# Kernel tuning notes

Hardware: AMD Instinct MI355X
Metric: run time of the kernel (lower is better)

The kernel has to match this reference:

```python
import jax, jax.numpy as jnp
import numpy as np
from jax import lax

ALPHA = 1.5
DIM = -1
N_ITER = 50


def entmax_bisect(x, alpha=ALPHA, dim=DIM, n_iter=N_ITER):
    # alpha == 1.0 would reduce to softmax; alpha is a static Python float here.
    if alpha == 1.0:
        return jax.nn.softmax(x, axis=dim)
    am1 = alpha - 1.0
    z = x - jnp.max(x, axis=dim, keepdims=True)          # max(z) == 0 along dim
    am1_z = am1 * z
    # torch code sorts z and takes the top element; that equals max(z) == 0, so
    # hi = 0 and lo = hi - 1. We compute the max directly (same math, no sort).
    hi = jnp.max(am1_z, axis=dim, keepdims=True)          # == 0
    lo = hi - 1.0

    inv_am1 = 1.0 / am1

    def sum_probs(tau):
        # sum_i max(0, am1*z_i - tau)^{1/am1}, keepdims
        diff = jnp.maximum(am1_z - tau, 0.0)
        return jnp.sum(jnp.power(diff, inv_am1), axis=dim, keepdims=True)

    # The torch version expands lo downward (up to 64 times) until
    # sum_probs(lo) >= 1 everywhere. Since max(am1_z) == hi, at lo = hi - 1 the
    # argmax element alone contributes (hi - lo)^{1/am1} = 1^{1/am1} = 1, so
    # sum_probs(lo) >= 1 always holds and the torch loop breaks on the first
    # iteration without ever modifying lo. We therefore skip it (identical math).

    def bisect_step(carry, _):
        lo, hi = carry
        mid = (lo + hi) * 0.5
        s = sum_probs(mid)
        lo = jnp.where(s > 1.0, mid, lo)
        hi = jnp.where(s <= 1.0, mid, hi)
        return (lo, hi), None

    (lo, hi), _ = lax.scan(bisect_step, (lo, hi), None, length=n_iter)
    tau_star = (lo + hi) * 0.5
    p = jnp.power(jnp.maximum(am1_z - tau_star, 0.0), inv_am1)
    return p / jnp.maximum(jnp.sum(p, axis=dim, keepdims=True), 1e-12)


def setup_inputs() -> dict:
    key = jax.random.key(0)
    x = jax.random.normal(key, (8, 2048, 2048), dtype=jnp.float32)
    return {"x": x}


def reference(x):
    return entmax_bisect(x, alpha=ALPHA, dim=DIM, n_iter=N_ITER)
```

## Files before the change

### kernel.cpp

```cpp
#include <hip/hip_runtime.h>


typedef float f32x4 __attribute__((ext_vector_type(4)));

constexpr int N = 2048;
constexpr int PER_LANE = N / 64;
constexpr int WPB = 4;
constexpr int CAPL = 12;
constexpr int BMAX = 8;
constexpr int K1 = 6;
constexpr int TOTAL_ITER = 50;

__device__ __forceinline__ float wave_sum(float s) {
    #pragma unroll
    for (int off = 32; off >= 1; off >>= 1)
        s += __shfl_xor(s, off, 64);
    return s;
}
__device__ __forceinline__ float wave_max(float m) {
    #pragma unroll
    for (int off = 32; off >= 1; off >>= 1)
        m = fmaxf(m, __shfl_xor(m, off, 64));
    return m;
}

__global__ __launch_bounds__(256, 6)
void entmax15_kernel(const float* __restrict__ x,
                     float* __restrict__ out, int rows) {
    __shared__ float s_cand[WPB][CAPL][64];
    __shared__ float s_bnd[WPB][BMAX];
    __shared__ int   s_cnt[WPB];

    const int wave = threadIdx.x >> 6;
    const int lane = threadIdx.x & 63;
    const int row  = blockIdx.x * WPB + wave;
    if (row >= rows) return;

    const f32x4* xr   = reinterpret_cast<const f32x4*>(x + (size_t)row * N);
    f32x4*       outr = reinterpret_cast<f32x4*>(out + (size_t)row * N);

    float v[PER_LANE];
    #pragma unroll
    for (int c = 0; c < PER_LANE / 4; ++c) {
        f32x4 t = xr[lane + 64 * c];
        v[4*c+0] = t.x; v[4*c+1] = t.y; v[4*c+2] = t.z; v[4*c+3] = t.w;
    }

    float m = v[0];
    #pragma unroll
    for (int i = 1; i < PER_LANE; ++i) m = fmaxf(m, v[i]);
    m = wave_max(m);

    const float nhm = -0.5f * m;
    #pragma unroll
    for (int i = 0; i < PER_LANE; ++i) v[i] = fmaf(0.5f, v[i], nhm);

    #pragma unroll
    for (int k = 0; k < CAPL; ++k) s_cand[wave][k][lane] = -1e30f;
    if (lane < BMAX) s_bnd[wave][lane] = -1e30f;
    if (lane == 0)   s_cnt[wave] = 0;

    int j = 0;
    #pragma unroll
    for (int i = 0; i < PER_LANE; ++i) {
        const bool cand = v[i] > -1.0f;
        const int  slot = (j < CAPL - 1) ? j : (CAPL - 1);
        if (cand) s_cand[wave][slot][lane] = v[i];
        j += cand ? 1 : 0;
    }

    float tau, ssum;
    if (!__any(j > CAPL)) {
        float cd[CAPL];
        #pragma unroll
        for (int k = 0; k < CAPL; ++k) cd[k] = s_cand[wave][k][lane];

        float lo = -1.0f, hi = 0.0f;
        for (int it = 0; it < K1; ++it) {
            const float mid = 0.5f * (lo + hi);
            float sa = 0.f, sb = 0.f;
            #pragma unroll
            for (int k = 0; k < CAPL; k += 2) {
                float d0 = fmaxf(cd[k]   - mid, 0.f);
                float d1 = fmaxf(cd[k+1] - mid, 0.f);
                sa = fmaf(d0, d0, sa);
                sb = fmaf(d1, d1, sb);
            }
            float s = wave_sum(sa + sb);
            if (s > 1.0f) lo = mid; else hi = mid;
        }

        const float cth = hi, lof = lo;
        float nA = 0.f, S1 = 0.f, S2 = 0.f;
        #pragma unroll
        for (int k = 0; k < CAPL; ++k) {
            float u  = cd[k] - cth;
            float um = fmaxf(u, 0.f);
            nA += (u > 0.f) ? 1.0f : 0.0f;
            S1 += um;
            S2  = fmaf(um, um, S2);
            if (u <= 0.f && cd[k] > lof) {
                int t = atomicAdd(&s_cnt[wave], 1);
                if (t < BMAX) s_bnd[wave][t] = cd[k];
            }
        }
        nA = wave_sum(nA); S1 = wave_sum(S1); S2 = wave_sum(S2);

        const int cnt = s_cnt[wave];
        if (cnt <= BMAX) {
            float b0 = s_bnd[wave][0], b1 = s_bnd[wave][1];
            float b2 = s_bnd[wave][2], b3 = s_bnd[wave][3];
            float b4 = s_bnd[wave][4], b5 = s_bnd[wave][5];
            float b6 = s_bnd[wave][6], b7 = s_bnd[wave][7];
            #define CE(a, b) { float _t = fmaxf(a, b); b = fminf(a, b); a = _t; }
            CE(b0,b1) CE(b2,b3) CE(b4,b5) CE(b6,b7)
            CE(b0,b2) CE(b1,b3) CE(b4,b6) CE(b5,b7)
            CE(b1,b2) CE(b5,b6)
            CE(b0,b4) CE(b1,b5) CE(b2,b6) CE(b3,b7)
            CE(b2,b4) CE(b3,b5)
            CE(b1,b2) CE(b3,b4) CE(b5,b6)
            #undef CE
            float nk = nA, S1k = S1, S2k = S2;
            #define STEP(bk) {                                              \
                float t_  = bk - cth;                                       \
                float sc_ = fmaf(t_, fmaf(nk, t_, -2.0f * S1k), S2k);       \
                bool  ac_ = sc_ < 1.0f;                                     \
                float ta_ = ac_ ? t_ : 0.0f;                                \
                nk  += ac_ ? 1.0f : 0.0f;                                   \
                S1k += ta_;                                                 \
                S2k  = fmaf(ta_, ta_, S2k); }
            STEP(b0) STEP(b1) STEP(b2) STEP(b3)
            STEP(b4) STEP(b5) STEP(b6) STEP(b7)
            #undef STEP
            float disc = fmaxf(fmaf(S1k, S1k, -nk * (S2k - 1.0f)), 0.0f);
            tau = cth + (S1k - sqrtf(disc)) / nk;
        } else {
            for (int it = 0; it < TOTAL_ITER - K1; ++it) {
                const float mid = 0.5f * (lo + hi);
                float sa = 0.f, sb = 0.f;
                #pragma unroll
                for (int k = 0; k < CAPL; k += 2) {
                    float d0 = fmaxf(cd[k]   - mid, 0.f);
                    float d1 = fmaxf(cd[k+1] - mid, 0.f);
                    sa = fmaf(d0, d0, sa);
                    sb = fmaf(d1, d1, sb);
                }
                float s = wave_sum(sa + sb);
                if (s > 1.0f) lo = mid; else hi = mid;
            }
            tau = 0.5f * (lo + hi);
        }

        float sa = 0.f, sb = 0.f;
        #pragma unroll
        for (int k = 0; k < CAPL; k += 2) {
            float d0 = fmaxf(cd[k]   - tau, 0.f);
            float d1 = fmaxf(cd[k+1] - tau, 0.f);
            sa = fmaf(d0, d0, sa);
            sb = fmaf(d1, d1, sb);
        }
        ssum = wave_sum(sa + sb);
    } else {
        float lo = -1.0f, hi = 0.0f;
        for (int it = 0; it < TOTAL_ITER; ++it) {
            const float mid = 0.5f * (lo + hi);
            float s0 = 0.f, s1_ = 0.f, s2_ = 0.f, s3_ = 0.f;
            #pragma unroll
            for (int i = 0; i < PER_LANE; i += 4) {
                float d0 = fmaxf(v[i+0] - mid, 0.f);
                float d1 = fmaxf(v[i+1] - mid, 0.f);
                float d2 = fmaxf(v[i+2] - mid, 0.f);
                float d3 = fmaxf(v[i+3] - mid, 0.f);
                s0 = fmaf(d0, d0, s0); s1_ = fmaf(d1, d1, s1_);
                s2_ = fmaf(d2, d2, s2_); s3_ = fmaf(d3, d3, s3_);
            }
            float s = wave_sum((s0 + s1_) + (s2_ + s3_));
            if (s > 1.0f) lo = mid; else hi = mid;
        }
        tau = 0.5f * (lo + hi);
        float s0 = 0.f;
        #pragma unroll
        for (int i = 0; i < PER_LANE; ++i) {
            float d = fmaxf(v[i] - tau, 0.f);
            s0 = fmaf(d, d, s0);
        }
        ssum = wave_sum(s0);
    }

    const float inv = 1.0f / fmaxf(ssum, 1e-12f);
    #pragma unroll
    for (int c = 0; c < PER_LANE / 4; ++c) {
        float d0 = fmaxf(v[4*c+0] - tau, 0.f);
        float d1 = fmaxf(v[4*c+1] - tau, 0.f);
        float d2 = fmaxf(v[4*c+2] - tau, 0.f);
        float d3 = fmaxf(v[4*c+3] - tau, 0.f);
        f32x4 t;
        t.x = (d0 * d0) * inv;
        t.y = (d1 * d1) * inv;
        t.z = (d2 * d2) * inv;
        t.w = (d3 * d3) * inv;
        __builtin_nontemporal_store(t, &outr[lane + 64 * c]);
    }
}

extern "C" void kernel_launch(void* const* d_in, const int* in_sizes, int n_in,
                              void* d_out, int out_size, void* d_ws, size_t ws_size,
                              hipStream_t stream) {
    const float* x = (const float*)d_in[0];
    float* out = (float*)d_out;
    const int rows = in_sizes[0] / N;
    const int blocks = (rows + WPB - 1) / WPB;
    entmax15_kernel<<<blocks, 64 * WPB, 0, stream>>>(x, out, rows);
}
```

Baseline: 57.75 us.

## Process several rows per wave with register prefetch of the next row

Each wave now handles RPW rows strided across the grid and issues the global loads for the next row into registers before solving the current one. The goal is to overlap HBM load latency with the threshold-solve compute, instead of relying only on occupancy. This adds 32 prefetch registers per lane, and launch bounds drop from 6 to 4 blocks per CU, which lowers occupancy. The grid shrinks by a factor of four.

```diff
diff --git a/kernel.cpp b/kernel.cpp
--- a/kernel.cpp
+++ b/kernel.cpp
@@ -6,6 +6,7 @@
 constexpr int N = 2048;
 constexpr int PER_LANE = N / 64;
 constexpr int WPB = 4;
+constexpr int RPW = 4;
 constexpr int CAPL = 12;
 constexpr int BMAX = 8;
 constexpr int K1 = 6;
@@ -24,56 +25,29 @@
     return m;
 }
 
-__global__ __launch_bounds__(256, 6)
-void entmax15_kernel(const float* __restrict__ x,
-                     float* __restrict__ out, int rows) {
-    __shared__ float s_cand[WPB][CAPL][64];
-    __shared__ float s_bnd[WPB][BMAX];
-    __shared__ int   s_cnt[WPB];
-
-    const int wave = threadIdx.x >> 6;
-    const int lane = threadIdx.x & 63;
-    const int row  = blockIdx.x * WPB + wave;
-    if (row >= rows) return;
-
-    const f32x4* xr   = reinterpret_cast<const f32x4*>(x + (size_t)row * N);
-    f32x4*       outr = reinterpret_cast<f32x4*>(out + (size_t)row * N);
-
-    float v[PER_LANE];
-    #pragma unroll
-    for (int c = 0; c < PER_LANE / 4; ++c) {
-        f32x4 t = xr[lane + 64 * c];
-        v[4*c+0] = t.x; v[4*c+1] = t.y; v[4*c+2] = t.z; v[4*c+3] = t.w;
-    }
-
-    float m = v[0];
-    #pragma unroll
-    for (int i = 1; i < PER_LANE; ++i) m = fmaxf(m, v[i]);
-    m = wave_max(m);
-
-    const float nhm = -0.5f * m;
-    #pragma unroll
-    for (int i = 0; i < PER_LANE; ++i) v[i] = fmaf(0.5f, v[i], nhm);
-
-    #pragma unroll
-    for (int k = 0; k < CAPL; ++k) s_cand[wave][k][lane] = -1e30f;
-    if (lane < BMAX) s_bnd[wave][lane] = -1e30f;
-    if (lane == 0)   s_cnt[wave] = 0;
+__device__ __forceinline__ void solve_and_store(
+        float (&v)[PER_LANE], f32x4* __restrict__ outr, int lane,
+        float (&cand)[CAPL][64], float (&bnd)[BMAX], int* cntp) {
+
+    #pragma unroll
+    for (int k = 0; k < CAPL; ++k) cand[k][lane] = -1e30f;
+    if (lane < BMAX) bnd[lane] = -1e30f;
+    if (lane == 0)   *cntp = 0;
 
     int j = 0;
     #pragma unroll
     for (int i = 0; i < PER_LANE; ++i) {
-        const bool cand = v[i] > -1.0f;
+        const bool c = v[i] > -1.0f;
         const int  slot = (j < CAPL - 1) ? j : (CAPL - 1);
-        if (cand) s_cand[wave][slot][lane] = v[i];
-        j += cand ? 1 : 0;
+        if (c) cand[slot][lane] = v[i];
+        j += c ? 1 : 0;
     }
 
     float tau, ssum;
     if (!__any(j > CAPL)) {
         float cd[CAPL];
         #pragma unroll
-        for (int k = 0; k < CAPL; ++k) cd[k] = s_cand[wave][k][lane];
+        for (int k = 0; k < CAPL; ++k) cd[k] = cand[k][lane];
 
         float lo = -1.0f, hi = 0.0f;
         for (int it = 0; it < K1; ++it) {
@@ -100,18 +74,16 @@
             S1 += um;
             S2  = fmaf(um, um, S2);
             if (u <= 0.f && cd[k] > lof) {
-                int t = atomicAdd(&s_cnt[wave], 1);
-                if (t < BMAX) s_bnd[wave][t] = cd[k];
+                int t = atomicAdd(cntp, 1);
+                if (t < BMAX) bnd[t] = cd[k];
             }
         }
         nA = wave_sum(nA); S1 = wave_sum(S1); S2 = wave_sum(S2);
 
-        const int cnt = s_cnt[wave];
+        const int cnt = *cntp;
         if (cnt <= BMAX) {
-            float b0 = s_bnd[wave][0], b1 = s_bnd[wave][1];
-            float b2 = s_bnd[wave][2], b3 = s_bnd[wave][3];
-            float b4 = s_bnd[wave][4], b5 = s_bnd[wave][5];
-            float b6 = s_bnd[wave][6], b7 = s_bnd[wave][7];
+            float b0 = bnd[0], b1 = bnd[1], b2 = bnd[2], b3 = bnd[3];
+            float b4 = bnd[4], b5 = bnd[5], b6 = bnd[6], b7 = bnd[7];
             #define CE(a, b) { float _t = fmaxf(a, b); b = fminf(a, b); a = _t; }
             CE(b0,b1) CE(b2,b3) CE(b4,b5) CE(b6,b7)
             CE(b0,b2) CE(b1,b3) CE(b4,b6) CE(b5,b7)
@@ -203,12 +175,67 @@
     }
 }
 
+__global__ __launch_bounds__(256, 4)
+void entmax15_kernel(const float* __restrict__ x,
+                     float* __restrict__ out, int rows) {
+    __shared__ float s_cand[WPB][CAPL][64];
+    __shared__ float s_bnd[WPB][BMAX];
+    __shared__ int   s_cnt[WPB];
+
+    const int wave = threadIdx.x >> 6;
+    const int lane = threadIdx.x & 63;
+    const int gw   = blockIdx.x * WPB + wave;
+    const int nwaves = gridDim.x * WPB;
+
+    f32x4 pf[8];
+    {
+        const f32x4* xr = reinterpret_cast<const f32x4*>(x + (size_t)gw * N);
+        #pragma unroll
+        for (int c = 0; c < 8; ++c) pf[c] = xr[lane + 64 * c];
+    }
+
+    #pragma unroll
+    for (int k = 0; k < RPW; ++k) {
+        const int row = gw + k * nwaves;
+        if (row >= rows) return;
+
+        float m = fmaxf(fmaxf(pf[0].x, pf[0].y), fmaxf(pf[0].z, pf[0].w));
+        #pragma unroll
+        for (int c = 1; c < 8; ++c)
+            m = fmaxf(m, fmaxf(fmaxf(pf[c].x, pf[c].y), fmaxf(pf[c].z, pf[c].w)));
+        m = wave_max(m);
+
+        const float nhm = -0.5f * m;
+        float v[PER_LANE];
+        #pragma unroll
+        for (int c = 0; c < 8; ++c) {
+            v[4*c+0] = fmaf(0.5f, pf[c].x, nhm);
+            v[4*c+1] = fmaf(0.5f, pf[c].y, nhm);
+            v[4*c+2] = fmaf(0.5f, pf[c].z, nhm);
+            v[4*c+3] = fmaf(0.5f, pf[c].w, nhm);
+        }
+
+        if (k + 1 < RPW) {
+            const int nrow = gw + (k + 1) * nwaves;
+            if (nrow < rows) {
+                const f32x4* xr = reinterpret_cast<const f32x4*>(x + (size_t)nrow * N);
+                #pragma unroll
+                for (int c = 0; c < 8; ++c) pf[c] = xr[lane + 64 * c];
+            }
+        }
+
+        f32x4* outr = reinterpret_cast<f32x4*>(out + (size_t)row * N);
+        solve_and_store(v, outr, lane, s_cand[wave], s_bnd[wave], &s_cnt[wave]);
+    }
+}
+
 extern "C" void kernel_launch(void* const* d_in, const int* in_sizes, int n_in,
                               void* d_out, int out_size, void* d_ws, size_t ws_size,
                               hipStream_t stream) {
     const float* x = (const float*)d_in[0];
     float* out = (float*)d_out;
     const int rows = in_sizes[0] / N;
-    const int blocks = (rows + WPB - 1) / WPB;
+    const int nwaves = (rows + RPW - 1) / RPW;
+    const int blocks = (nwaves + WPB - 1) / WPB;
     entmax15_kernel<<<blocks, 64 * WPB, 0, stream>>>(x, out, rows);
 }
```

Result: slower. 72.62 us (+25.7%).

## Process two rows per wavefront to interleave independent reductions

Applied to the files above, without the earlier changes.

Each wavefront now handles two rows, interleaving their loads, max reductions, candidate bisection, shuffle reductions and stores so the two independent dependency chains can hide each other's latency. Launch bounds drop from 6 to 4 blocks per CU to make room for the doubled register footprint, and the nontemporal stores become ordinary stores. If either row overflows the candidate buffer, both rows take the full 50-iteration fallback. This risks register pressure and lower occupancy, and it assumes an even row count.

```diff
diff --git a/kernel.cpp b/kernel.cpp
--- a/kernel.cpp
+++ b/kernel.cpp
@@ -17,177 +17,33 @@
         s += __shfl_xor(s, off, 64);
     return s;
 }
-__device__ __forceinline__ float wave_max(float m) {
-    #pragma unroll
-    for (int off = 32; off >= 1; off >>= 1)
-        m = fmaxf(m, __shfl_xor(m, off, 64));
-    return m;
-}
-
-__global__ __launch_bounds__(256, 6)
-void entmax15_kernel(const float* __restrict__ x,
-                     float* __restrict__ out, int rows) {
-    __shared__ float s_cand[WPB][CAPL][64];
-    __shared__ float s_bnd[WPB][BMAX];
-    __shared__ int   s_cnt[WPB];
-
-    const int wave = threadIdx.x >> 6;
-    const int lane = threadIdx.x & 63;
-    const int row  = blockIdx.x * WPB + wave;
-    if (row >= rows) return;
-
-    const f32x4* xr   = reinterpret_cast<const f32x4*>(x + (size_t)row * N);
-    f32x4*       outr = reinterpret_cast<f32x4*>(out + (size_t)row * N);
-
-    float v[PER_LANE];
-    #pragma unroll
-    for (int c = 0; c < PER_LANE / 4; ++c) {
-        f32x4 t = xr[lane + 64 * c];
-        v[4*c+0] = t.x; v[4*c+1] = t.y; v[4*c+2] = t.z; v[4*c+3] = t.w;
-    }
-
-    float m = v[0];
-    #pragma unroll
-    for (int i = 1; i < PER_LANE; ++i) m = fmaxf(m, v[i]);
-    m = wave_max(m);
-
-    const float nhm = -0.5f * m;
-    #pragma unroll
-    for (int i = 0; i < PER_LANE; ++i) v[i] = fmaf(0.5f, v[i], nhm);
-
-    #pragma unroll
-    for (int k = 0; k < CAPL; ++k) s_cand[wave][k][lane] = -1e30f;
-    if (lane < BMAX) s_bnd[wave][lane] = -1e30f;
-    if (lane == 0)   s_cnt[wave] = 0;
-
-    int j = 0;
+
+__device__ __forceinline__ void full_solve_store(
+        float (&v)[PER_LANE], f32x4* __restrict__ outr, int lane) {
+    float lo = -1.0f, hi = 0.0f;
+    for (int it = 0; it < TOTAL_ITER; ++it) {
+        const float mid = 0.5f * (lo + hi);
+        float s0 = 0.f, s1 = 0.f, s2 = 0.f, s3 = 0.f;
+        #pragma unroll
+        for (int i = 0; i < PER_LANE; i += 4) {
+            float d0 = fmaxf(v[i+0] - mid, 0.f);
+            float d1 = fmaxf(v[i+1] - mid, 0.f);
+            float d2 = fmaxf(v[i+2] - mid, 0.f);
+            float d3 = fmaxf(v[i+3] - mid, 0.f);
+            s0 = fmaf(d0, d0, s0); s1 = fmaf(d1, d1, s1);
+            s2 = fmaf(d2, d2, s2); s3 = fmaf(d3, d3, s3);
+        }
+        float s = wave_sum((s0 + s1) + (s2 + s3));
+        if (s > 1.0f) lo = mid; else hi = mid;
+    }
+    const float tau = 0.5f * (lo + hi);
+    float s0 = 0.f;
     #pragma unroll
     for (int i = 0; i < PER_LANE; ++i) {
-        const bool cand = v[i] > -1.0f;
-        const int  slot = (j < CAPL - 1) ? j : (CAPL - 1);
-        if (cand) s_cand[wave][slot][lane] = v[i];
-        j += cand ? 1 : 0;
-    }
-
-    float tau, ssum;
-    if (!__any(j > CAPL)) {
-        float cd[CAPL];
-        #pragma unroll
-        for (int k = 0; k < CAPL; ++k) cd[k] = s_cand[wave][k][lane];
-
-        float lo = -1.0f, hi = 0.0f;
-        for (int it = 0; it < K1; ++it) {
-            const float mid = 0.5f * (lo + hi);
-            float sa = 0.f, sb = 0.f;
-            #pragma unroll
-            for (int k = 0; k < CAPL; k += 2) {
-                float d0 = fmaxf(cd[k]   - mid, 0.f);
-                float d1 = fmaxf(cd[k+1] - mid, 0.f);
-                sa = fmaf(d0, d0, sa);
-                sb = fmaf(d1, d1, sb);
-            }
-            float s = wave_sum(sa + sb);
-            if (s > 1.0f) lo = mid; else hi = mid;
-        }
-
-        const float cth = hi, lof = lo;
-        float nA = 0.f, S1 = 0.f, S2 = 0.f;
-        #pragma unroll
-        for (int k = 0; k < CAPL; ++k) {
-            float u  = cd[k] - cth;
-            float um = fmaxf(u, 0.f);
-            nA += (u > 0.f) ? 1.0f : 0.0f;
-            S1 += um;
-            S2  = fmaf(um, um, S2);
-            if (u <= 0.f && cd[k] > lof) {
-                int t = atomicAdd(&s_cnt[wave], 1);
-                if (t < BMAX) s_bnd[wave][t] = cd[k];
-            }
-        }
-        nA = wave_sum(nA); S1 = wave_sum(S1); S2 = wave_sum(S2);
-
-        const int cnt = s_cnt[wave];
-        if (cnt <= BMAX) {
-            float b0 = s_bnd[wave][0], b1 = s_bnd[wave][1];
-            float b2 = s_bnd[wave][2], b3 = s_bnd[wave][3];
-            float b4 = s_bnd[wave][4], b5 = s_bnd[wave][5];
-            float b6 = s_bnd[wave][6], b7 = s_bnd[wave][7];
-            #define CE(a, b) { float _t = fmaxf(a, b); b = fminf(a, b); a = _t; }
-            CE(b0,b1) CE(b2,b3) CE(b4,b5) CE(b6,b7)
-            CE(b0,b2) CE(b1,b3) CE(b4,b6) CE(b5,b7)
-            CE(b1,b2) CE(b5,b6)
-            CE(b0,b4) CE(b1,b5) CE(b2,b6) CE(b3,b7)
-            CE(b2,b4) CE(b3,b5)
-            CE(b1,b2) CE(b3,b4) CE(b5,b6)
-            #undef CE
-            float nk = nA, S1k = S1, S2k = S2;
-            #define STEP(bk) {                                              \
-                float t_  = bk - cth;                                       \
-                float sc_ = fmaf(t_, fmaf(nk, t_, -2.0f * S1k), S2k);       \
-                bool  ac_ = sc_ < 1.0f;                                     \
-                float ta_ = ac_ ? t_ : 0.0f;                                \
-                nk  += ac_ ? 1.0f : 0.0f;                                   \
-                S1k += ta_;                                                 \
-                S2k  = fmaf(ta_, ta_, S2k); }
-            STEP(b0) STEP(b1) STEP(b2) STEP(b3)
-            STEP(b4) STEP(b5) STEP(b6) STEP(b7)
-            #undef STEP
-            float disc = fmaxf(fmaf(S1k, S1k, -nk * (S2k - 1.0f)), 0.0f);
-            tau = cth + (S1k - sqrtf(disc)) / nk;
-        } else {
-            for (int it = 0; it < TOTAL_ITER - K1; ++it) {
-                const float mid = 0.5f * (lo + hi);
-                float sa = 0.f, sb = 0.f;
-                #pragma unroll
-                for (int k = 0; k < CAPL; k += 2) {
-                    float d0 = fmaxf(cd[k]   - mid, 0.f);
-                    float d1 = fmaxf(cd[k+1] - mid, 0.f);
-                    sa = fmaf(d0, d0, sa);
-                    sb = fmaf(d1, d1, sb);
-                }
-                float s = wave_sum(sa + sb);
-                if (s > 1.0f) lo = mid; else hi = mid;
-            }
-            tau = 0.5f * (lo + hi);
-        }
-
-        float sa = 0.f, sb = 0.f;
-        #pragma unroll
-        for (int k = 0; k < CAPL; k += 2) {
-            float d0 = fmaxf(cd[k]   - tau, 0.f);
-            float d1 = fmaxf(cd[k+1] - tau, 0.f);
-            sa = fmaf(d0, d0, sa);
-            sb = fmaf(d1, d1, sb);
-        }
-        ssum = wave_sum(sa + sb);
-    } else {
-        float lo = -1.0f, hi = 0.0f;
-        for (int it = 0; it < TOTAL_ITER; ++it) {
-            const float mid = 0.5f * (lo + hi);
-            float s0 = 0.f, s1_ = 0.f, s2_ = 0.f, s3_ = 0.f;
-            #pragma unroll
-            for (int i = 0; i < PER_LANE; i += 4) {
-                float d0 = fmaxf(v[i+0] - mid, 0.f);
-                float d1 = fmaxf(v[i+1] - mid, 0.f);
-                float d2 = fmaxf(v[i+2] - mid, 0.f);
-                float d3 = fmaxf(v[i+3] - mid, 0.f);
-                s0 = fmaf(d0, d0, s0); s1_ = fmaf(d1, d1, s1_);
-                s2_ = fmaf(d2, d2, s2_); s3_ = fmaf(d3, d3, s3_);
-            }
-            float s = wave_sum((s0 + s1_) + (s2_ + s3_));
-            if (s > 1.0f) lo = mid; else hi = mid;
-        }
-        tau = 0.5f * (lo + hi);
-        float s0 = 0.f;
-        #pragma unroll
-        for (int i = 0; i < PER_LANE; ++i) {
-            float d = fmaxf(v[i] - tau, 0.f);
-            s0 = fmaf(d, d, s0);
-        }
-        ssum = wave_sum(s0);
-    }
-
-    const float inv = 1.0f / fmaxf(ssum, 1e-12f);
+        float d = fmaxf(v[i] - tau, 0.f);
+        s0 = fmaf(d, d, s0);
+    }
+    const float inv = 1.0f / fmaxf(wave_sum(s0), 1e-12f);
     #pragma unroll
     for (int c = 0; c < PER_LANE / 4; ++c) {
         float d0 = fmaxf(v[4*c+0] - tau, 0.f);
@@ -195,11 +51,247 @@
         float d2 = fmaxf(v[4*c+2] - tau, 0.f);
         float d3 = fmaxf(v[4*c+3] - tau, 0.f);
         f32x4 t;
-        t.x = (d0 * d0) * inv;
-        t.y = (d1 * d1) * inv;
-        t.z = (d2 * d2) * inv;
-        t.w = (d3 * d3) * inv;
-        __builtin_nontemporal_store(t, &outr[lane + 64 * c]);
+        t.x = (d0*d0)*inv; t.y = (d1*d1)*inv;
+        t.z = (d2*d2)*inv; t.w = (d3*d3)*inv;
+        outr[lane + 64 * c] = t;
+    }
+}
+
+__device__ __forceinline__ float closed_form_tau(
+        const float* bnd, float cth, float nA, float S1, float S2) {
+    float b0 = bnd[0], b1 = bnd[1], b2 = bnd[2], b3 = bnd[3];
+    float b4 = bnd[4], b5 = bnd[5], b6 = bnd[6], b7 = bnd[7];
+    #define CE(a, b) { float _t = fmaxf(a, b); b = fminf(a, b); a = _t; }
+    CE(b0,b1) CE(b2,b3) CE(b4,b5) CE(b6,b7)
+    CE(b0,b2) CE(b1,b3) CE(b4,b6) CE(b5,b7)
+    CE(b1,b2) CE(b5,b6)
+    CE(b0,b4) CE(b1,b5) CE(b2,b6) CE(b3,b7)
+    CE(b2,b4) CE(b3,b5)
+    CE(b1,b2) CE(b3,b4) CE(b5,b6)
+    #undef CE
+    float nk = nA, S1k = S1, S2k = S2;
+    #define STEP(bk) {                                              \
+        float t_  = bk - cth;                                       \
+        float sc_ = fmaf(t_, fmaf(nk, t_, -2.0f * S1k), S2k);       \
+        bool  ac_ = sc_ < 1.0f;                                     \
+        float ta_ = ac_ ? t_ : 0.0f;                                \
+        nk  += ac_ ? 1.0f : 0.0f;                                   \
+        S1k += ta_;                                                 \
+        S2k  = fmaf(ta_, ta_, S2k); }
+    STEP(b0) STEP(b1) STEP(b2) STEP(b3)
+    STEP(b4) STEP(b5) STEP(b6) STEP(b7)
+    #undef STEP
+    float disc = fmaxf(fmaf(S1k, S1k, -nk * (S2k - 1.0f)), 0.0f);
+    return cth + (S1k - sqrtf(disc)) / nk;
+}
+
+__device__ __forceinline__ float bisect_tail_tau(
+        float (&cd)[CAPL], float lo, float hi) {
+    for (int it = 0; it < TOTAL_ITER - K1; ++it) {
+        const float mid = 0.5f * (lo + hi);
+        float sa = 0.f, sb = 0.f;
+        #pragma unroll
+        for (int k = 0; k < CAPL; k += 2) {
+            float d0 = fmaxf(cd[k]   - mid, 0.f);
+            float d1 = fmaxf(cd[k+1] - mid, 0.f);
+            sa = fmaf(d0, d0, sa);
+            sb = fmaf(d1, d1, sb);
+        }
+        float s = wave_sum(sa + sb);
+        if (s > 1.0f) lo = mid; else hi = mid;
+    }
+    return 0.5f * (lo + hi);
+}
+
+__global__ __launch_bounds__(256, 4)
+void entmax15_kernel(const float* __restrict__ x,
+                     float* __restrict__ out, int rows) {
+    __shared__ float s_cand[WPB][2][CAPL][64];
+    __shared__ float s_bnd[WPB][2][BMAX];
+    __shared__ int   s_cnt[WPB][2];
+
+    const int wave = threadIdx.x >> 6;
+    const int lane = threadIdx.x & 63;
+    const int gw   = blockIdx.x * WPB + wave;
+    const int rowA = 2 * gw;
+    const int rowB = rowA + 1;
+    if (rowA >= rows) return;
+
+    const f32x4* xA = reinterpret_cast<const f32x4*>(x + (size_t)rowA * N);
+    const f32x4* xB = reinterpret_cast<const f32x4*>(x + (size_t)rowB * N);
+    f32x4* outA = reinterpret_cast<f32x4*>(out + (size_t)rowA * N);
+    f32x4* outB = reinterpret_cast<f32x4*>(out + (size_t)rowB * N);
+
+    float vA[PER_LANE], vB[PER_LANE];
+    #pragma unroll
+    for (int c = 0; c < 8; ++c) {
+        f32x4 t = xA[lane + 64 * c];
+        vA[4*c+0] = t.x; vA[4*c+1] = t.y; vA[4*c+2] = t.z; vA[4*c+3] = t.w;
+    }
+    #pragma unroll
+    for (int c = 0; c < 8; ++c) {
+        f32x4 t = xB[lane + 64 * c];
+        vB[4*c+0] = t.x; vB[4*c+1] = t.y; vB[4*c+2] = t.z; vB[4*c+3] = t.w;
+    }
+
+    float mA = vA[0], mB = vB[0];
+    #pragma unroll
+    for (int i = 1; i < PER_LANE; ++i) {
+        mA = fmaxf(mA, vA[i]);
+        mB = fmaxf(mB, vB[i]);
+    }
+    #pragma unroll
+    for (int off = 32; off >= 1; off >>= 1) {
+        mA = fmaxf(mA, __shfl_xor(mA, off, 64));
+        mB = fmaxf(mB, __shfl_xor(mB, off, 64));
+    }
+
+    const float nhA = -0.5f * mA, nhB = -0.5f * mB;
+    #pragma unroll
+    for (int i = 0; i < PER_LANE; ++i) {
+        vA[i] = fmaf(0.5f, vA[i], nhA);
+        vB[i] = fmaf(0.5f, vB[i], nhB);
+    }
+
+    #pragma unroll
+    for (int k = 0; k < CAPL; ++k) {
+        s_cand[wave][0][k][lane] = -1e30f;
+        s_cand[wave][1][k][lane] = -1e30f;
+    }
+    if (lane < BMAX) { s_bnd[wave][0][lane] = -1e30f; s_bnd[wave][1][lane] = -1e30f; }
+    if (lane == 0)   { s_cnt[wave][0] = 0; s_cnt[wave][1] = 0; }
+
+    int jA = 0, jB = 0;
+    #pragma unroll
+    for (int i = 0; i < PER_LANE; ++i) {
+        const bool cA = vA[i] > -1.0f;
+        const int  sA = (jA < CAPL - 1) ? jA : (CAPL - 1);
+        if (cA) s_cand[wave][0][sA][lane] = vA[i];
+        jA += cA ? 1 : 0;
+        const bool cB = vB[i] > -1.0f;
+        const int  sB = (jB < CAPL - 1) ? jB : (CAPL - 1);
+        if (cB) s_cand[wave][1][sB][lane] = vB[i];
+        jB += cB ? 1 : 0;
+    }
+
+    if (__any((jA > CAPL) || (jB > CAPL))) {
+        full_solve_store(vA, outA, lane);
+        full_solve_store(vB, outB, lane);
+        return;
+    }
+
+    float cdA[CAPL], cdB[CAPL];
+    #pragma unroll
+    for (int k = 0; k < CAPL; ++k) {
+        cdA[k] = s_cand[wave][0][k][lane];
+        cdB[k] = s_cand[wave][1][k][lane];
+    }
+
+    float loA = -1.0f, hiA = 0.0f, loB = -1.0f, hiB = 0.0f;
+    #pragma unroll
+    for (int it = 0; it < K1; ++it) {
+        const float midA = 0.5f * (loA + hiA);
+        const float midB = 0.5f * (loB + hiB);
+        float a0 = 0.f, a1 = 0.f, b0 = 0.f, b1 = 0.f;
+        #pragma unroll
+        for (int k = 0; k < CAPL; k += 2) {
+            float dA0 = fmaxf(cdA[k]   - midA, 0.f);
+            float dA1 = fmaxf(cdA[k+1] - midA, 0.f);
+            float dB0 = fmaxf(cdB[k]   - midB, 0.f);
+            float dB1 = fmaxf(cdB[k+1] - midB, 0.f);
+            a0 = fmaf(dA0, dA0, a0); a1 = fmaf(dA1, dA1, a1);
+            b0 = fmaf(dB0, dB0, b0); b1 = fmaf(dB1, dB1, b1);
+        }
+        float sA = a0 + a1, sB = b0 + b1;
+        #pragma unroll
+        for (int off = 32; off >= 1; off >>= 1) {
+            sA += __shfl_xor(sA, off, 64);
+            sB += __shfl_xor(sB, off, 64);
+        }
+        loA = (sA > 1.0f) ? midA : loA;  hiA = (sA > 1.0f) ? hiA : midA;
+        loB = (sB > 1.0f) ? midB : loB;  hiB = (sB > 1.0f) ? hiB : midB;
+    }
+
+    const float cthA = hiA, lofA = loA, cthB = hiB, lofB = loB;
+    float nAa = 0.f, S1a = 0.f, S2a = 0.f;
+    float nAb = 0.f, S1b = 0.f, S2b = 0.f;
+    #pragma unroll
+    for (int k = 0; k < CAPL; ++k) {
+        float uA  = cdA[k] - cthA;
+        float umA = fmaxf(uA, 0.f);
+        nAa += (uA > 0.f) ? 1.0f : 0.0f;
+        S1a += umA;
+        S2a  = fmaf(umA, umA, S2a);
+        if (uA <= 0.f && cdA[k] > lofA) {
+            int t = atomicAdd(&s_cnt[wave][0], 1);
+            if (t < BMAX) s_bnd[wave][0][t] = cdA[k];
+        }
+        float uB  = cdB[k] - cthB;
+        float umB = fmaxf(uB, 0.f);
+        nAb += (uB > 0.f) ? 1.0f : 0.0f;
+        S1b += umB;
+        S2b  = fmaf(umB, umB, S2b);
+        if (uB <= 0.f && cdB[k] > lofB) {
+            int t = atomicAdd(&s_cnt[wave][1], 1);
+            if (t < BMAX) s_bnd[wave][1][t] = cdB[k];
+        }
+    }
+    #pragma unroll
+    for (int off = 32; off >= 1; off >>= 1) {
+        nAa += __shfl_xor(nAa, off, 64);
+        S1a += __shfl_xor(S1a, off, 64);
+        S2a += __shfl_xor(S2a, off, 64);
+        nAb += __shfl_xor(nAb, off, 64);
+        S1b += __shfl_xor(S1b, off, 64);
+        S2b += __shfl_xor(S2b, off, 64);
+    }
+
+    const int cntA = s_cnt[wave][0];
+    const int cntB = s_cnt[wave][1];
+
+    float tauA = (cntA <= BMAX)
+        ? closed_form_tau(s_bnd[wave][0], cthA, nAa, S1a, S2a)
+        : bisect_tail_tau(cdA, loA, hiA);
+    float tauB = (cntB <= BMAX)
+        ? closed_form_tau(s_bnd[wave][1], cthB, nAb, S1b, S2b)
+        : bisect_tail_tau(cdB, loB, hiB);
+
+    float a0 = 0.f, a1 = 0.f, b0 = 0.f, b1 = 0.f;
+    #pragma unroll
+    for (int k = 0; k < CAPL; k += 2) {
+        float dA0 = fmaxf(cdA[k]   - tauA, 0.f);
+        float dA1 = fmaxf(cdA[k+1] - tauA, 0.f);
+        float dB0 = fmaxf(cdB[k]   - tauB, 0.f);
+        float dB1 = fmaxf(cdB[k+1] - tauB, 0.f);
+        a0 = fmaf(dA0, dA0, a0); a1 = fmaf(dA1, dA1, a1);
+        b0 = fmaf(dB0, dB0, b0); b1 = fmaf(dB1, dB1, b1);
+    }
+    float ssA = a0 + a1, ssB = b0 + b1;
+    #pragma unroll
+    for (int off = 32; off >= 1; off >>= 1) {
+        ssA += __shfl_xor(ssA, off, 64);
+        ssB += __shfl_xor(ssB, off, 64);
+    }
+    const float invA = 1.0f / fmaxf(ssA, 1e-12f);
+    const float invB = 1.0f / fmaxf(ssB, 1e-12f);
+
+    #pragma unroll
+    for (int c = 0; c < PER_LANE / 4; ++c) {
+        float dA0 = fmaxf(vA[4*c+0] - tauA, 0.f);
+        float dA1 = fmaxf(vA[4*c+1] - tauA, 0.f);
+        float dA2 = fmaxf(vA[4*c+2] - tauA, 0.f);
+        float dA3 = fmaxf(vA[4*c+3] - tauA, 0.f);
+        f32x4 t;
+        t.x = (dA0*dA0)*invA; t.y = (dA1*dA1)*invA;
+        t.z = (dA2*dA2)*invA; t.w = (dA3*dA3)*invA;
+        outA[lane + 64 * c] = t;
+        float dB0 = fmaxf(vB[4*c+0] - tauB, 0.f);
+        float dB1 = fmaxf(vB[4*c+1] - tauB, 0.f);
+        float dB2 = fmaxf(vB[4*c+2] - tauB, 0.f);
+        float dB3 = fmaxf(vB[4*c+3] - tauB, 0.f);
+        t.x = (dB0*dB0)*invB; t.y = (dB1*dB1)*invB;
+        t.z = (dB2*dB2)*invB; t.w = (dB3*dB3)*invB;
+        outB[lane + 64 * c] = t;
     }
 }
 
@@ -209,6 +301,7 @@
     const float* x = (const float*)d_in[0];
     float* out = (float*)d_out;
     const int rows = in_sizes[0] / N;
-    const int blocks = (rows + WPB - 1) / WPB;
+    const int pairs = rows / 2;
+    const int blocks = (pairs + WPB - 1) / WPB;
     entmax15_kernel<<<blocks, 64 * WPB, 0, stream>>>(x, out, rows);
 }
```

Result: slower. 88.91 us (+53.9%).
